# Kernel optimization log

Measured on AMD Instinct MI355X. Metric: run time of the kernel, lower is better.

## Reference

```python
import jax, jax.numpy as jnp
import numpy as np

B = 1
DIM = 2048
N_HEADS = 16
HEAD_DIM = 128
RANK = 128
ALPHA = 128.0
L_NOISE = 2048
L_COND = 1024
N_LORAS = 1
EPS = 1e-6
NEG = -1e20


def setup_inputs() -> dict:
    key = jax.random.key(0)
    ks = jax.random.split(key, 24)
    inp = {}
    inp["noise_flat"] = jax.random.normal(ks[0], (B, L_NOISE, DIM), jnp.float32)
    inp["cond_flat"] = jax.random.normal(ks[1], (B, L_COND, DIM), jnp.float32)
    # RoPE freqs in TE 'bshd' convention: (L, head_dim), halves duplicated
    inv_freq = 1.0 / (10000.0 ** (jnp.arange(0, HEAD_DIM, 2, dtype=jnp.float32) / HEAD_DIM))
    pos = jnp.arange(L_NOISE + L_COND, dtype=jnp.float32)
    fr = pos[:, None] * inv_freq[None, :]
    fr = jnp.concatenate([fr, fr], axis=-1)  # (L, HEAD_DIM)
    inp["noise_rope"] = fr[:L_NOISE]
    inp["cond_rope"] = fr[L_NOISE:]
    std = 0.02
    inp["Wq"] = jax.random.normal(ks[2], (DIM, DIM), jnp.float32) * std
    inp["Wk"] = jax.random.normal(ks[3], (DIM, DIM), jnp.float32) * std
    inp["Wv"] = jax.random.normal(ks[4], (DIM, DIM), jnp.float32) * std
    inp["Wo"] = jax.random.normal(ks[5], (DIM, DIM), jnp.float32) * std
    inp["bq"] = jnp.zeros((DIM,), jnp.float32)
    inp["bk"] = jnp.zeros((DIM,), jnp.float32)
    inp["bv"] = jnp.zeros((DIM,), jnp.float32)
    inp["bo"] = jnp.zeros((DIM,), jnp.float32)
    inp["q_norm_scale"] = jnp.ones((HEAD_DIM,), jnp.float32)
    inp["k_norm_scale"] = jnp.ones((HEAD_DIM,), jnp.float32)
    inp["v_norm_scale"] = jnp.ones((HEAD_DIM,), jnp.float32)
    # LoRA: down ~ N(0, 1/rank); up small nonzero (torch inits zeros, made nonzero for a meaningful baseline)
    for name, ki in zip(["q", "k", "v", "o"], range(6, 10)):
        k1, k2 = jax.random.split(ks[ki])
        inp[f"lora_{name}_down"] = jax.random.normal(k1, (DIM, RANK), jnp.float32) / RANK
        inp[f"lora_{name}_up"] = jax.random.normal(k2, (RANK, DIM), jnp.float32) * 0.01
    return inp


def _rms_norm(x, scale):
    return x * jax.lax.rsqrt(jnp.mean(x * x, axis=-1, keepdims=True) + EPS) * scale


def _rotate_half(x):
    x1, x2 = jnp.split(x, 2, axis=-1)
    return jnp.concatenate([-x2, x1], axis=-1)


def _apply_rope(x, freqs):
    # x: (B, L, H, D), freqs: (L, D)
    cos = jnp.cos(freqs)[None, :, None, :]
    sin = jnp.sin(freqs)[None, :, None, :]
    return x * cos + _rotate_half(x) * sin


def _block_mask():
    # noise rows attend to everything; cond block i attends only to itself
    L = L_NOISE + L_COND * N_LORAS
    idx = jnp.arange(L)
    is_noise = idx < L_NOISE
    blk = (idx - L_NOISE) // L_COND
    allowed = is_noise[:, None] | (
        (~is_noise[:, None]) & (~is_noise[None, :]) & (blk[:, None] == blk[None, :])
    )
    return jnp.where(allowed, 0.0, NEG).astype(jnp.float32)  # (L, L)


def _cond_mask(i, L):
    idx = jnp.arange(L)
    start = L_NOISE + i * L_COND
    return ((idx >= start) & (idx < start + L_COND)).astype(jnp.float32)[None, :, None]


def reference(noise_flat, cond_flat, noise_rope, cond_rope,
              Wq, Wk, Wv, Wo, bq, bk, bv, bo,
              q_norm_scale, k_norm_scale, v_norm_scale,
              lora_q_down, lora_q_up, lora_k_down, lora_k_up,
              lora_v_down, lora_v_up, lora_o_down, lora_o_up):
    joint = jnp.concatenate([noise_flat, cond_flat], axis=1)  # (B, L, D)
    rope = jnp.concatenate([noise_rope, cond_rope], axis=0)   # (L, HEAD_DIM)
    L = joint.shape[1]
    scale_lora = ALPHA / RANK
    m = _cond_mask(0, L)  # n_loras = 1, lora_weight = 1.0
    jm = joint * m

    def lora(x_masked, Wd, Wu):
        return (x_masked @ Wd) @ Wu * scale_lora

    q = joint @ Wq + bq + lora(jm, lora_q_down, lora_q_up)
    k = joint @ Wk + bk + lora(jm, lora_k_down, lora_k_up)
    v = joint @ Wv + bv + lora(jm, lora_v_down, lora_v_up)

    q = q.reshape(B, L, N_HEADS, HEAD_DIM)
    k = k.reshape(B, L, N_HEADS, HEAD_DIM)
    v = v.reshape(B, L, N_HEADS, HEAD_DIM)
    q = _rms_norm(q, q_norm_scale)
    k = _rms_norm(k, k_norm_scale)
    v = _rms_norm(v, v_norm_scale)
    q = _apply_rope(q, rope)
    k = _apply_rope(k, rope)

    bias = _block_mask()[None, None]  # (1,1,L,L)
    scores = jnp.einsum('bqhd,bkhd->bhqk', q, k) / jnp.sqrt(jnp.float32(HEAD_DIM)) + bias
    attn = jax.nn.softmax(scores, axis=-1)
    x = jnp.einsum('bhqk,bkhd->bqhd', attn, v).reshape(B, L, DIM)

    out = x @ Wo + bo + lora(x * m, lora_o_down, lora_o_up)
    return out[:, :L_NOISE, :], out[:, L_NOISE:, :]
```

## Files before the change

### kernel.cpp

```cpp
#include <hip/hip_runtime.h>

typedef _Float16 f16;
typedef _Float16 half8 __attribute__((ext_vector_type(8)));
typedef float floatx4 __attribute__((ext_vector_type(4)));

#define L_TOT   3072
#define L_NZ    2048
#define DIM_C   2048
#define NH      16
#define HD      128

__device__ __forceinline__ void gl_lds16(const f16* g, f16* l) {
    __builtin_amdgcn_global_load_lds((__attribute__((address_space(1))) void*)g,
                                     (__attribute__((address_space(3))) void*)l,
                                     16, 0, 0);
}

__global__ void sentinel_kernel(float* out) { out[0] = 1.0e6f; }

__global__ __launch_bounds__(256)
void cast_joint(const float* __restrict__ noise, const float* __restrict__ cond,
                f16* __restrict__ out) {
    int i = (blockIdx.x * 256 + threadIdx.x) * 4;
    const float* src; int off;
    if (i < 2048 * 2048) { src = noise; off = i; }
    else                 { src = cond;  off = i - 2048 * 2048; }
    float4 v = *(const float4*)(src + off);
    out[i+0] = (f16)v.x; out[i+1] = (f16)v.y;
    out[i+2] = (f16)v.z; out[i+3] = (f16)v.w;
}

__global__ __launch_bounds__(256)
void transpose_cast4(const float* __restrict__ s0, const float* __restrict__ s1,
                     const float* __restrict__ s2, const float* __restrict__ s3,
                     f16* __restrict__ dstBase, int R, int C, long long outBatch) {
    const float* in = (blockIdx.z == 0) ? s0 : (blockIdx.z == 1) ? s1 : (blockIdx.z == 2) ? s2 : s3;
    f16* out = dstBase + (long long)blockIdx.z * outBatch;
    __shared__ f16 tile[32][33];
    int x = threadIdx.x & 31, y0 = threadIdx.x >> 5;
    int r0 = blockIdx.y * 32, c0 = blockIdx.x * 32;
#pragma unroll
    for (int i = 0; i < 4; ++i) {
        int y = y0 + i * 8;
        tile[y][x] = (f16)in[(size_t)(r0 + y) * C + (c0 + x)];
    }
    __syncthreads();
#pragma unroll
    for (int i = 0; i < 4; ++i) {
        int y = y0 + i * 8;
        out[(size_t)(c0 + y) * R + (r0 + x)] = tile[x][y];
    }
}

template<int WRITE_HALF, int ACCUM, int ADD_BIAS, int MODE>
__global__ __launch_bounds__(256, 2)
void gemm_tn(const f16* __restrict__ A, const f16* __restrict__ BT,
             void* __restrict__ Cv,
             const float* __restrict__ bias0,
             int M, int N, int K, int lda, int ldb, int ldc) {
    __shared__ __align__(16) f16 lds[2][2][128 * 64];
    const int tid  = threadIdx.x;
    const int lane = tid & 63, wave = tid >> 6;
    const int m0 = blockIdx.y * 128, n0 = blockIdx.x * 128;
    const int wr = wave >> 1, wc = wave & 1;
    floatx4 acc[4][4] = {};

    if (MODE == 2) A += (size_t)(n0 >> 11) * 128;

    const int r0i = tid >> 3;
    const int gch = (tid & 7) ^ (r0i & 7);
    const f16* gA0 = A  + (size_t)(m0 + r0i) * lda + gch * 8;
    const f16* gB0 = BT + (size_t)(n0 + r0i) * ldb + gch * 8;
    const int ldsW = wave * 512;

    auto stage = [&](int buf, int k0) {
#pragma unroll
        for (int is = 0; is < 4; ++is)
            gl_lds16(gA0 + k0 + (size_t)is * 32 * lda, &lds[buf][0][0] + is * 2048 + ldsW);
#pragma unroll
        for (int is = 0; is < 4; ++is)
            gl_lds16(gB0 + k0 + (size_t)is * 32 * ldb, &lds[buf][1][0] + is * 2048 + ldsW);
    };

    const int rl = lane & 15, cq = lane >> 4;

    const int nIter = K >> 6;
    stage(0, 0);
    int cur = 0;
    for (int t = 0; t < nIter; ++t) {
        const int k0n = (t + 1 < nIter) ? (t + 1) * 64 : 0;
        stage(cur ^ 1, k0n);
        asm volatile("s_waitcnt vmcnt(8)" ::: "memory");
        __builtin_amdgcn_s_barrier();
        __builtin_amdgcn_sched_barrier(0);
#pragma unroll
        for (int kh = 0; kh < 2; ++kh) {
            half8 af[4], bf[4];
#pragma unroll
            for (int m = 0; m < 4; ++m) {
                int row = wr * 64 + m * 16 + rl;
                int pos = (kh * 4 + cq) ^ (row & 7);
                af[m] = *(const half8*)(&lds[cur][0][row * 64 + pos * 8]);
            }
#pragma unroll
            for (int n = 0; n < 4; ++n) {
                int row = wc * 64 + n * 16 + rl;
                int pos = (kh * 4 + cq) ^ (row & 7);
                bf[n] = *(const half8*)(&lds[cur][1][row * 64 + pos * 8]);
            }
#pragma unroll
            for (int m = 0; m < 4; ++m)
#pragma unroll
                for (int n = 0; n < 4; ++n)
                    acc[m][n] = __builtin_amdgcn_mfma_f32_16x16x32_f16(af[m], bf[n], acc[m][n], 0, 0, 0);
        }
        __builtin_amdgcn_s_barrier();
        __builtin_amdgcn_sched_barrier(0);
        cur ^= 1;
    }

    const int rq = lane >> 4;
    size_t cbase = 0;
    if (MODE == 2) cbase = (size_t)(n0 >> 11) * ((size_t)L_TOT * DIM_C);
#pragma unroll
    for (int m = 0; m < 4; ++m) {
        int row = m0 + wr * 64 + m * 16 + rq * 4;
#pragma unroll
        for (int n = 0; n < 4; ++n) {
            int col = n0 + wc * 64 + n * 16 + rl;
            int ccol = (MODE == 2) ? (col & 2047) : col;
            float badd = ADD_BIAS ? bias0[ccol] : 0.0f;
#pragma unroll
            for (int j = 0; j < 4; ++j) {
                float v = acc[m][n][j] + badd;
                size_t idx = cbase + (size_t)(row + j) * ldc + ccol;
                if (WRITE_HALF) {
                    f16* C = (f16*)Cv;
                    if (ACCUM) v += (float)C[idx];
                    C[idx] = (f16)v;
                } else {
                    float* C = (float*)Cv;
                    if (ACCUM) v += C[idx];
                    C[idx] = v;
                }
            }
        }
    }
}

__global__ __launch_bounds__(256, 2)
void gemm_pair(int nb0, int nbx0,
               const f16* __restrict__ A0, const f16* __restrict__ BT0, void* C0,
               const float* __restrict__ b00, const float* __restrict__ b01, const float* __restrict__ b02,
               int lda0, int ldb0, int ldc0, int wh0, int ab0, int mode0,
               int nbx1,
               const f16* __restrict__ A1, const f16* __restrict__ BT1, void* C1,
               int lda1, int ldb1, int ldc1, int wh1,
               int K) {
    __shared__ __align__(16) f16 lds[2][2][128 * 64];
    const int tid  = threadIdx.x;
    const int lane = tid & 63, wave = tid >> 6;
    const int bid = blockIdx.x;
    const bool j0 = (bid < nb0);
    const int lb  = j0 ? bid : (bid - nb0);
    const int nbx = j0 ? nbx0 : nbx1;
    const int bx = lb % nbx, by = lb / nbx;
    const int m0 = by * 128, n0 = bx * 128;
    const f16* A  = j0 ? A0  : A1;
    const f16* BT = j0 ? BT0 : BT1;
    const int lda = j0 ? lda0 : lda1, ldb = j0 ? ldb0 : ldb1, ldc = j0 ? ldc0 : ldc1;
    const int wr = wave >> 1, wc = wave & 1;
    floatx4 acc[4][4] = {};

    const int r0i = tid >> 3;
    const int gch = (tid & 7) ^ (r0i & 7);
    const f16* gA0 = A  + (size_t)(m0 + r0i) * lda + gch * 8;
    const f16* gB0 = BT + (size_t)(n0 + r0i) * ldb + gch * 8;
    const int ldsW = wave * 512;

    auto stage = [&](int buf, int k0) {
#pragma unroll
        for (int is = 0; is < 4; ++is)
            gl_lds16(gA0 + k0 + (size_t)is * 32 * lda, &lds[buf][0][0] + is * 2048 + ldsW);
#pragma unroll
        for (int is = 0; is < 4; ++is)
            gl_lds16(gB0 + k0 + (size_t)is * 32 * ldb, &lds[buf][1][0] + is * 2048 + ldsW);
    };

    const int rl = lane & 15, cq = lane >> 4;
    const int nIter = K >> 6;
    stage(0, 0);
    int cur = 0;
    for (int t = 0; t < nIter; ++t) {
        const int k0n = (t + 1 < nIter) ? (t + 1) * 64 : 0;
        stage(cur ^ 1, k0n);
        asm volatile("s_waitcnt vmcnt(8)" ::: "memory");
        __builtin_amdgcn_s_barrier();
        __builtin_amdgcn_sched_barrier(0);
#pragma unroll
        for (int kh = 0; kh < 2; ++kh) {
            half8 af[4], bf[4];
#pragma unroll
            for (int m = 0; m < 4; ++m) {
                int row = wr * 64 + m * 16 + rl;
                int pos = (kh * 4 + cq) ^ (row & 7);
                af[m] = *(const half8*)(&lds[cur][0][row * 64 + pos * 8]);
            }
#pragma unroll
            for (int n = 0; n < 4; ++n) {
                int row = wc * 64 + n * 16 + rl;
                int pos = (kh * 4 + cq) ^ (row & 7);
                bf[n] = *(const half8*)(&lds[cur][1][row * 64 + pos * 8]);
            }
#pragma unroll
            for (int m = 0; m < 4; ++m)
#pragma unroll
                for (int n = 0; n < 4; ++n)
                    acc[m][n] = __builtin_amdgcn_mfma_f32_16x16x32_f16(af[m], bf[n], acc[m][n], 0, 0, 0);
        }
        __builtin_amdgcn_s_barrier();
        __builtin_amdgcn_sched_barrier(0);
        cur ^= 1;
    }

    const int rq = lane >> 4;
    const int wh = j0 ? wh0 : wh1;
    const int ab = j0 ? ab0 : 0;
    const int md = j0 ? mode0 : 0;
    void* Cv = j0 ? C0 : C1;
    size_t cbase = 0;
    const float* bias = b00;
    if (md == 1) {
        int chunk = n0 >> 11;
        bias = (chunk == 0) ? b00 : ((chunk == 1) ? b01 : b02);
        cbase = (size_t)chunk * ((size_t)L_TOT * DIM_C);
    }
#pragma unroll
    for (int m = 0; m < 4; ++m) {
        int row = m0 + wr * 64 + m * 16 + rq * 4;
#pragma unroll
        for (int n = 0; n < 4; ++n) {
            int col = n0 + wc * 64 + n * 16 + rl;
            int ccol = (md == 1) ? (col & 2047) : col;
            float badd = ab ? bias[ccol] : 0.0f;
#pragma unroll
            for (int j = 0; j < 4; ++j) {
                float v = acc[m][n][j] + badd;
                size_t idx = cbase + (size_t)(row + j) * ldc + ccol;
                if (wh) ((f16*)Cv)[idx] = (f16)v;
                else    ((float*)Cv)[idx] = v;
            }
        }
    }
}

__global__ __launch_bounds__(256)
void norm_rope_v(const f16* __restrict__ q16, const f16* __restrict__ k16, const f16* __restrict__ v16,
                 const float* __restrict__ qs, const float* __restrict__ ks, const float* __restrict__ vs,
                 const float* __restrict__ nrope, const float* __restrict__ crope,
                 f16* __restrict__ qH, f16* __restrict__ kH, f16* __restrict__ vT) {
    __shared__ f16 vtile[128][33];
    const int t = threadIdx.x, rloc = t >> 3, c = t & 7;
    const int r = blockIdx.x * 32 + rloc, h = blockIdx.y;
    const int d0 = c * 8;
    const size_t src = (size_t)r * DIM_C + h * HD;
    half8 qlv = *(const half8*)(q16 + src + d0);
    half8 qhv = *(const half8*)(q16 + src + 64 + d0);
    half8 klv = *(const half8*)(k16 + src + d0);
    half8 khv = *(const half8*)(k16 + src + 64 + d0);
    half8 vlv = *(const half8*)(v16 + src + d0);
    half8 vhv = *(const half8*)(v16 + src + 64 + d0);
    float ql[8], qh[8], kl[8], kh[8], vl[8], vh[8];
    float sq = 0.f, sk = 0.f, sv = 0.f;
#pragma unroll
    for (int i = 0; i < 8; ++i) {
        ql[i] = (float)qlv[i]; qh[i] = (float)qhv[i];
        kl[i] = (float)klv[i]; kh[i] = (float)khv[i];
        vl[i] = (float)vlv[i]; vh[i] = (float)vhv[i];
        sq += ql[i]*ql[i] + qh[i]*qh[i];
        sk += kl[i]*kl[i] + kh[i]*kh[i];
        sv += vl[i]*vl[i] + vh[i]*vh[i];
    }
    sq += __shfl_xor(sq, 1); sq += __shfl_xor(sq, 2); sq += __shfl_xor(sq, 4);
    sk += __shfl_xor(sk, 1); sk += __shfl_xor(sk, 2); sk += __shfl_xor(sk, 4);
    sv += __shfl_xor(sv, 1); sv += __shfl_xor(sv, 2); sv += __shfl_xor(sv, 4);
    const float rqs = rsqrtf(sq * (1.0f / 128.0f) + 1e-6f);
    const float rks = rsqrtf(sk * (1.0f / 128.0f) + 1e-6f);
    const float rvs = rsqrtf(sv * (1.0f / 128.0f) + 1e-6f);
    const float* rp = (r < L_NZ) ? (nrope + (size_t)r * HD) : (crope + (size_t)(r - L_NZ) * HD);
    half8 qo_l, qo_h, ko_l, ko_h;
#pragma unroll
    for (int i = 0; i < 8; ++i) {
        float fr = rp[d0 + i];
        float cs = cosf(fr), sn = sinf(fr);
        float qnl = ql[i] * rqs * qs[d0 + i],      qnh = qh[i] * rqs * qs[64 + d0 + i];
        float knl = kl[i] * rks * ks[d0 + i],      knh = kh[i] * rks * ks[64 + d0 + i];
        qo_l[i] = (f16)((qnl * cs - qnh * sn) * 0.08838834764831845f);
        qo_h[i] = (f16)((qnh * cs + qnl * sn) * 0.08838834764831845f);
        ko_l[i] = (f16)(knl * cs - knh * sn);
        ko_h[i] = (f16)(knh * cs + knl * sn);
        vtile[d0 + i][rloc]      = (f16)(vl[i] * rvs * vs[d0 + i]);
        vtile[64 + d0 + i][rloc] = (f16)(vh[i] * rvs * vs[64 + d0 + i]);
    }
    const size_t dst = ((size_t)h * L_TOT + r) * HD;
    *(half8*)(qH + dst + d0) = qo_l;      *(half8*)(qH + dst + 64 + d0) = qo_h;
    *(half8*)(kH + dst + d0) = ko_l;      *(half8*)(kH + dst + 64 + d0) = ko_h;
    __syncthreads();
    const int dd = t >> 1, seg = (t & 1) * 16;
    half8 o0, o1;
#pragma unroll
    for (int i = 0; i < 8; ++i) { o0[i] = vtile[dd][seg + i]; o1[i] = vtile[dd][seg + 8 + i]; }
    f16* vdst = vT + ((size_t)h * HD + dd) * L_TOT + blockIdx.x * 32 + seg;
    *(half8*)(vdst)     = o0;
    *(half8*)(vdst + 8) = o1;
}

__global__ __launch_bounds__(256, 2)
void flash_kernel(const f16* __restrict__ qH, const f16* __restrict__ kH,
                  const f16* __restrict__ vT, f16* __restrict__ xH) {
    __shared__ __align__(16) f16 lds_k[2][64 * 128];
    __shared__ __align__(16) f16 lds_v[64 * 128];
    __shared__ __align__(16) f16 p_lds[4][16][72];
    const int tid = threadIdx.x;
    const int lane = tid & 63, w = tid >> 6;
    const int bid = blockIdx.x;
    const int xcd = bid & 7, rr = bid >> 3;
    int h, qb;
    if (rr < 32) { h = xcd + 8 * (rr >> 4); qb = 32 + (rr & 15); }
    else         { int li = rr - 32; h = xcd + 8 * (li >> 5); qb = li & 31; }
    const int q0 = qb * 64 + w * 16;
    const int rl = lane & 15, rq = lane >> 4;

    half8 aq[4];
    const f16* qbase = qH + ((size_t)h * L_TOT + q0) * HD;
#pragma unroll
    for (int kc = 0; kc < 4; ++kc)
        aq[kc] = *(const half8*)(qbase + (size_t)rl * HD + kc * 32 + rq * 8);

    floatx4 acc[8] = {};
    floatx4 accl = {};
    const half8 vone = {(f16)1.f, (f16)1.f, (f16)1.f, (f16)1.f,
                        (f16)1.f, (f16)1.f, (f16)1.f, (f16)1.f};

    const int kLo = (qb >= 32) ? L_NZ : 0;
    const f16* khead = kH + (size_t)h * L_TOT * HD;
    const f16* vhead = vT + (size_t)h * HD * L_TOT;

    auto stageK = [&](int kb, int pb) {
#pragma unroll
        for (int is = 0; is < 4; ++is) {
            int i = is * 256 + tid;
            int r = i >> 4, c = i & 15;
            gl_lds16(khead + (size_t)(kb + r) * HD + ((c ^ (r & 15)) * 8),
                     &lds_k[pb][0] + (is * 256 + w * 64) * 8);
        }
    };
    auto stageV = [&](int kb) {
#pragma unroll
        for (int is = 0; is < 4; ++is) {
            int i = is * 256 + tid;
            int pair = i >> 4, c10 = i & 15;
            int g10 = c10 ^ (pair & 15);
            int d = pair * 2 + (g10 >> 3), kchunk = g10 & 7;
            gl_lds16(vhead + (size_t)d * L_TOT + kb + kchunk * 8,
                     lds_v + (is * 256 + w * 64) * 8);
        }
    };

    asm volatile("s_waitcnt vmcnt(0)" ::: "memory");
    stageK(kLo, 0);
    int p = 0;
    for (int kb = kLo; kb < L_TOT; kb += 64) {
        const int kbn = (kb + 64 < L_TOT) ? (kb + 64) : kLo;
        stageV(kb);
        stageK(kbn, p ^ 1);
        asm volatile("s_waitcnt vmcnt(8)" ::: "memory");
        __builtin_amdgcn_s_barrier();
        __builtin_amdgcn_sched_barrier(0);

        const f16* kbase = &lds_k[p][0];
        floatx4 sacc[4] = {};
        __builtin_amdgcn_s_setprio(1);
#pragma unroll
        for (int kf = 0; kf < 4; ++kf) {
            int r = kf * 16 + rl;
#pragma unroll
            for (int kc = 0; kc < 4; ++kc) {
                half8 bk = *(const half8*)(kbase + r * 128 + (((kc * 4 + rq) ^ (r & 15)) * 8));
                sacc[kf] = __builtin_amdgcn_mfma_f32_16x16x32_f16(aq[kc], bk, sacc[kf], 0, 0, 0);
            }
        }
        __builtin_amdgcn_s_setprio(0);
#pragma unroll
        for (int kf = 0; kf < 4; ++kf)
#pragma unroll
            for (int j = 0; j < 4; ++j) {
                float pv = __expf(sacc[kf][j] - 4.0f);
                p_lds[w][rq * 4 + j][kf * 16 + rl] = (f16)pv;
            }

        asm volatile("s_waitcnt vmcnt(4)" ::: "memory");
        __builtin_amdgcn_s_barrier();
        __builtin_amdgcn_sched_barrier(0);

        __builtin_amdgcn_s_setprio(1);
#pragma unroll
        for (int kc = 0; kc < 2; ++kc) {
            half8 ap = *(const half8*)(&p_lds[w][rl][kc * 32 + rq * 8]);
            accl = __builtin_amdgcn_mfma_f32_16x16x32_f16(ap, vone, accl, 0, 0, 0);
#pragma unroll
            for (int dt = 0; dt < 8; ++dt) {
                int d = dt * 16 + rl;
                int g10 = (d & 1) * 8 + kc * 4 + rq;
                half8 bv = *(const half8*)(lds_v + (d >> 1) * 128 + ((g10 ^ ((d >> 1) & 15)) * 8));
                acc[dt] = __builtin_amdgcn_mfma_f32_16x16x32_f16(ap, bv, acc[dt], 0, 0, 0);
            }
        }
        __builtin_amdgcn_s_setprio(0);
        __builtin_amdgcn_s_barrier();
        p ^= 1;
    }

#pragma unroll
    for (int j = 0; j < 4; ++j) {
        float li = 1.0f / accl[j];
        int row = q0 + rq * 4 + j;
#pragma unroll
        for (int dt = 0; dt < 8; ++dt)
            xH[(size_t)row * DIM_C + h * HD + dt * 16 + rl] = (f16)(acc[dt][j] * li);
    }
}

extern "C" void kernel_launch(void* const* d_in, const int* in_sizes, int n_in,
                              void* d_out, int out_size, void* d_ws, size_t ws_size,
                              hipStream_t stream) {
    const float* noise = (const float*)d_in[0];
    const float* cond  = (const float*)d_in[1];
    const float* nrope = (const float*)d_in[2];
    const float* crope = (const float*)d_in[3];
    const float* Wq = (const float*)d_in[4];
    const float* Wk = (const float*)d_in[5];
    const float* Wv = (const float*)d_in[6];
    const float* Wo = (const float*)d_in[7];
    const float* bq = (const float*)d_in[8];
    const float* bk = (const float*)d_in[9];
    const float* bv = (const float*)d_in[10];
    const float* bo = (const float*)d_in[11];
    const float* qs = (const float*)d_in[12];
    const float* ks = (const float*)d_in[13];
    const float* vs = (const float*)d_in[14];
    const float* lqd = (const float*)d_in[15];
    const float* lqu = (const float*)d_in[16];
    const float* lkd = (const float*)d_in[17];
    const float* lku = (const float*)d_in[18];
    const float* lvd = (const float*)d_in[19];
    const float* lvu = (const float*)d_in[20];
    const float* lod = (const float*)d_in[21];
    const float* lou = (const float*)d_in[22];
    (void)in_sizes; (void)n_in; (void)out_size;

    char* ws = (char*)d_ws;
    const size_t SZ_LD = (size_t)L_TOT * DIM_C * sizeof(f16);
    const size_t SZ_W  = (size_t)DIM_C * DIM_C * sizeof(f16);
    size_t o = 0;
    auto take = [&](size_t b) { size_t r = o; o += (b + 255) & ~(size_t)255; return r; };
    f16* jointH = (f16*)(ws + take(SZ_LD));
    f16* WTqkv  = (f16*)(ws + take(4 * SZ_W));
    f16* WT3    = WTqkv + (size_t)3 * 2048 * 2048;
    f16* downT  = (f16*)(ws + take((size_t)4 * 128 * 2048 * 2));
    f16* downTo = downT + (size_t)3 * 128 * 2048;
    f16* upT    = (f16*)(ws + take((size_t)4 * 2048 * 128 * 2));
    f16* upTo   = upT + (size_t)3 * 2048 * 128;
    f16* q16    = (f16*)(ws + take(3 * SZ_LD));
    f16* k16    = q16 + (size_t)L_TOT * DIM_C;
    f16* v16    = k16 + (size_t)L_TOT * DIM_C;
    f16* t_all  = (f16*)(ws + take((size_t)1024 * 384 * 2));
    f16* t_o    = (f16*)(ws + take((size_t)1024 * 128 * 2));
    f16* qHd    = (f16*)(ws + take(SZ_LD));
    f16* kHd    = (f16*)(ws + take(SZ_LD));
    f16* vTd    = (f16*)(ws + take(SZ_LD));
    f16* xH     = (f16*)(ws + take(SZ_LD));
    if (o > ws_size) {
        sentinel_kernel<<<1, 1, 0, stream>>>((float*)d_out);
        return;
    }

    cast_joint<<<dim3(6144), 256, 0, stream>>>(noise, cond, jointH);
    transpose_cast4<<<dim3(64, 64, 4), 256, 0, stream>>>(Wq, Wk, Wv, Wo, WTqkv, 2048, 2048,
                                                         (long long)2048 * 2048);
    transpose_cast4<<<dim3(4, 64, 4), 256, 0, stream>>>(lqd, lkd, lvd, lod, downT, 2048, 128,
                                                        (long long)128 * 2048);
    transpose_cast4<<<dim3(64, 4, 4), 256, 0, stream>>>(lqu, lku, lvu, lou, upT, 128, 2048,
                                                        (long long)2048 * 128);

    gemm_pair<<<dim3(1152 + 24), 256, 0, stream>>>(
        1152, 48, jointH, WTqkv, q16, bq, bk, bv, 2048, 2048, 2048, 1, 1, 1,
        3, jointH + (size_t)2048 * 2048, downT, t_all, 2048, 2048, 384, 1,
        2048);
    gemm_tn<1, 1, 0, 2><<<dim3(48, 8), 256, 0, stream>>>(t_all, upT, q16 + (size_t)2048 * 2048,
                                                         nullptr, 1024, 6144, 128, 384, 128, 2048);

    norm_rope_v<<<dim3(96, 16), 256, 0, stream>>>(q16, k16, v16, qs, ks, vs, nrope, crope,
                                                  qHd, kHd, vTd);

    flash_kernel<<<dim3(768), 256, 0, stream>>>(qHd, kHd, vTd, xH);

    gemm_pair<<<dim3(384 + 8), 256, 0, stream>>>(
        384, 16, xH, WT3, d_out, bo, nullptr, nullptr, 2048, 2048, 2048, 0, 1, 0,
        1, xH + (size_t)2048 * 2048, downTo, t_o, 2048, 2048, 128, 1,
        2048);
    gemm_tn<0, 1, 0, 0><<<dim3(16, 8), 256, 0, stream>>>(t_o, upTo, (float*)d_out + (size_t)2048 * 2048,
                                                         nullptr, 1024, 2048, 128, 128, 128, 2048);
}
```

Before: 338.4 us.

## Split noise-query attention over key ranges with partial outputs and a combine pass

The flash kernel now splits each noise query block's 3072-key range into three 1024-key slices. Each slice is handled by a separate workgroup, which writes a normalized partial output and its row sum. A new combine kernel merges the slices. Workgroups grow to 512 threads covering 128 query rows, with 32-key tiles and smaller LDS buffers, to balance the noise and cond workloads and raise occupancy. This adds a partial-output write and read through workspace (reusing the q16 buffer) and an extra launch, and it halves the per-iteration MFMA work relative to the sync overhead.

```diff
diff --git a/kernel.cpp b/kernel.cpp
--- a/kernel.cpp
+++ b/kernel.cpp
@@ -315,20 +315,25 @@
     *(half8*)(vdst + 8) = o1;
 }
 
-__global__ __launch_bounds__(256, 2)
+__global__ __launch_bounds__(512, 8)
 void flash_kernel(const f16* __restrict__ qH, const f16* __restrict__ kH,
-                  const f16* __restrict__ vT, f16* __restrict__ xH) {
-    __shared__ __align__(16) f16 lds_k[2][64 * 128];
-    __shared__ __align__(16) f16 lds_v[64 * 128];
-    __shared__ __align__(16) f16 p_lds[4][16][72];
+                  const f16* __restrict__ vT, f16* __restrict__ xH,
+                  f16* __restrict__ Opart, float* __restrict__ lpart) {
+    __shared__ __align__(16) f16 lds_k[2][32 * 128];
+    __shared__ __align__(16) f16 lds_v[64 * 64];
+    __shared__ __align__(16) f16 p_lds[8][16][40];
     const int tid = threadIdx.x;
     const int lane = tid & 63, w = tid >> 6;
     const int bid = blockIdx.x;
     const int xcd = bid & 7, rr = bid >> 3;
-    int h, qb;
-    if (rr < 32) { h = xcd + 8 * (rr >> 4); qb = 32 + (rr & 15); }
-    else         { int li = rr - 32; h = xcd + 8 * (li >> 5); qb = li & 31; }
-    const int q0 = qb * 64 + w * 16;
+    const int h = xcd + 8 * (rr / 56);
+    const int s = rr % 56;
+    const bool isNoise = (s < 48);
+    const int qb  = isNoise ? (s / 3) : (16 + (s - 48));
+    const int sl  = isNoise ? (s % 3) : 0;
+    const int kLo = isNoise ? sl * 1024 : L_NZ;
+    const int kHi = kLo + 1024;
+    const int q0 = qb * 128 + w * 16;
     const int rl = lane & 15, rq = lane >> 4;
 
     half8 aq[4];
@@ -342,47 +347,38 @@
     const half8 vone = {(f16)1.f, (f16)1.f, (f16)1.f, (f16)1.f,
                         (f16)1.f, (f16)1.f, (f16)1.f, (f16)1.f};
 
-    const int kLo = (qb >= 32) ? L_NZ : 0;
     const f16* khead = kH + (size_t)h * L_TOT * HD;
     const f16* vhead = vT + (size_t)h * HD * L_TOT;
 
     auto stageK = [&](int kb, int pb) {
-#pragma unroll
-        for (int is = 0; is < 4; ++is) {
-            int i = is * 256 + tid;
-            int r = i >> 4, c = i & 15;
-            gl_lds16(khead + (size_t)(kb + r) * HD + ((c ^ (r & 15)) * 8),
-                     &lds_k[pb][0] + (is * 256 + w * 64) * 8);
-        }
+        int r = tid >> 4, c = tid & 15;
+        gl_lds16(khead + (size_t)(kb + r) * HD + ((c ^ (r & 15)) * 8),
+                 &lds_k[pb][0] + tid * 8);
     };
     auto stageV = [&](int kb) {
-#pragma unroll
-        for (int is = 0; is < 4; ++is) {
-            int i = is * 256 + tid;
-            int pair = i >> 4, c10 = i & 15;
-            int g10 = c10 ^ (pair & 15);
-            int d = pair * 2 + (g10 >> 3), kchunk = g10 & 7;
-            gl_lds16(vhead + (size_t)d * L_TOT + kb + kchunk * 8,
-                     lds_v + (is * 256 + w * 64) * 8);
-        }
+        int pair = tid >> 3, c3 = tid & 7;
+        int g3 = c3 ^ (pair & 7);
+        int d = pair * 2 + (g3 >> 2), kchunk = g3 & 3;
+        gl_lds16(vhead + (size_t)d * L_TOT + kb + kchunk * 8,
+                 lds_v + tid * 8);
     };
 
     asm volatile("s_waitcnt vmcnt(0)" ::: "memory");
     stageK(kLo, 0);
     int p = 0;
-    for (int kb = kLo; kb < L_TOT; kb += 64) {
-        const int kbn = (kb + 64 < L_TOT) ? (kb + 64) : kLo;
+    for (int kb = kLo; kb < kHi; kb += 32) {
+        const int kbn = (kb + 32 < kHi) ? (kb + 32) : kLo;
         stageV(kb);
         stageK(kbn, p ^ 1);
-        asm volatile("s_waitcnt vmcnt(8)" ::: "memory");
+        asm volatile("s_waitcnt vmcnt(2)" ::: "memory");
         __builtin_amdgcn_s_barrier();
         __builtin_amdgcn_sched_barrier(0);
 
         const f16* kbase = &lds_k[p][0];
-        floatx4 sacc[4] = {};
+        floatx4 sacc[2] = {};
         __builtin_amdgcn_s_setprio(1);
 #pragma unroll
-        for (int kf = 0; kf < 4; ++kf) {
+        for (int kf = 0; kf < 2; ++kf) {
             int r = kf * 16 + rl;
 #pragma unroll
             for (int kc = 0; kc < 4; ++kc) {
@@ -392,43 +388,77 @@
         }
         __builtin_amdgcn_s_setprio(0);
 #pragma unroll
-        for (int kf = 0; kf < 4; ++kf)
+        for (int kf = 0; kf < 2; ++kf)
 #pragma unroll
             for (int j = 0; j < 4; ++j) {
                 float pv = __expf(sacc[kf][j] - 4.0f);
                 p_lds[w][rq * 4 + j][kf * 16 + rl] = (f16)pv;
             }
 
-        asm volatile("s_waitcnt vmcnt(4)" ::: "memory");
+        asm volatile("s_waitcnt vmcnt(1)" ::: "memory");
         __builtin_amdgcn_s_barrier();
         __builtin_amdgcn_sched_barrier(0);
 
+        half8 ap = *(const half8*)(&p_lds[w][rl][rq * 8]);
         __builtin_amdgcn_s_setprio(1);
-#pragma unroll
-        for (int kc = 0; kc < 2; ++kc) {
-            half8 ap = *(const half8*)(&p_lds[w][rl][kc * 32 + rq * 8]);
-            accl = __builtin_amdgcn_mfma_f32_16x16x32_f16(ap, vone, accl, 0, 0, 0);
-#pragma unroll
-            for (int dt = 0; dt < 8; ++dt) {
-                int d = dt * 16 + rl;
-                int g10 = (d & 1) * 8 + kc * 4 + rq;
-                half8 bv = *(const half8*)(lds_v + (d >> 1) * 128 + ((g10 ^ ((d >> 1) & 15)) * 8));
-                acc[dt] = __builtin_amdgcn_mfma_f32_16x16x32_f16(ap, bv, acc[dt], 0, 0, 0);
-            }
+        accl = __builtin_amdgcn_mfma_f32_16x16x32_f16(ap, vone, accl, 0, 0, 0);
+#pragma unroll
+        for (int dt = 0; dt < 8; ++dt) {
+            int d = dt * 16 + rl;
+            int pair = d >> 1;
+            int g3 = (d & 1) * 4 + rq;
+            half8 bv = *(const half8*)(lds_v + pair * 64 + ((g3 ^ (pair & 7)) * 8));
+            acc[dt] = __builtin_amdgcn_mfma_f32_16x16x32_f16(ap, bv, acc[dt], 0, 0, 0);
         }
         __builtin_amdgcn_s_setprio(0);
         __builtin_amdgcn_s_barrier();
         p ^= 1;
     }
 
-#pragma unroll
-    for (int j = 0; j < 4; ++j) {
-        float li = 1.0f / accl[j];
-        int row = q0 + rq * 4 + j;
-#pragma unroll
-        for (int dt = 0; dt < 8; ++dt)
-            xH[(size_t)row * DIM_C + h * HD + dt * 16 + rl] = (f16)(acc[dt][j] * li);
-    }
+    if (isNoise) {
+        f16* op = Opart + ((size_t)sl * NH + h) * ((size_t)L_NZ * HD);
+        float* lp = lpart + ((size_t)sl * NH + h) * L_NZ;
+#pragma unroll
+        for (int j = 0; j < 4; ++j) {
+            float li = 1.0f / accl[j];
+            int row = q0 + rq * 4 + j;
+            if (rl == 0) lp[row] = accl[j];
+#pragma unroll
+            for (int dt = 0; dt < 8; ++dt)
+                op[(size_t)row * HD + dt * 16 + rl] = (f16)(acc[dt][j] * li);
+        }
+    } else {
+#pragma unroll
+        for (int j = 0; j < 4; ++j) {
+            float li = 1.0f / accl[j];
+            int row = q0 + rq * 4 + j;
+#pragma unroll
+            for (int dt = 0; dt < 8; ++dt)
+                xH[(size_t)row * DIM_C + h * HD + dt * 16 + rl] = (f16)(acc[dt][j] * li);
+        }
+    }
+}
+
+__global__ __launch_bounds__(256)
+void combine_noise(const f16* __restrict__ Opart, const float* __restrict__ lpart,
+                   f16* __restrict__ xH) {
+    const size_t PS = (size_t)NH * L_NZ * HD;
+    const int t = threadIdx.x, lr = t >> 4, dc = t & 15;
+    const int R = blockIdx.x * 16 + lr;
+    const int h = R >> 11, q = R & 2047;
+    const float l0 = lpart[(size_t)0 * NH * L_NZ + (size_t)h * L_NZ + q];
+    const float l1 = lpart[(size_t)1 * NH * L_NZ + (size_t)h * L_NZ + q];
+    const float l2 = lpart[(size_t)2 * NH * L_NZ + (size_t)h * L_NZ + q];
+    const float inv = 1.0f / (l0 + l1 + l2);
+    const size_t base = ((size_t)h * L_NZ + q) * HD + dc * 8;
+    half8 a = *(const half8*)(Opart + 0 * PS + base);
+    half8 b = *(const half8*)(Opart + 1 * PS + base);
+    half8 c = *(const half8*)(Opart + 2 * PS + base);
+    half8 out;
+#pragma unroll
+    for (int i = 0; i < 8; ++i)
+        out[i] = (f16)((l0 * (float)a[i] + l1 * (float)b[i] + l2 * (float)c[i]) * inv);
+    *(half8*)(xH + (size_t)q * DIM_C + h * HD + dc * 8) = out;
 }
 
 extern "C" void kernel_launch(void* const* d_in, const int* in_sizes, int n_in,
@@ -480,6 +510,8 @@
     f16* kHd    = (f16*)(ws + take(SZ_LD));
     f16* vTd    = (f16*)(ws + take(SZ_LD));
     f16* xH     = (f16*)(ws + take(SZ_LD));
+    f16*   Opart = q16;
+    float* lpart = (float*)(q16 + (size_t)3 * NH * L_NZ * HD);
     if (o > ws_size) {
         sentinel_kernel<<<1, 1, 0, stream>>>((float*)d_out);
         return;
@@ -503,7 +535,8 @@
     norm_rope_v<<<dim3(96, 16), 256, 0, stream>>>(q16, k16, v16, qs, ks, vs, nrope, crope,
                                                   qHd, kHd, vTd);
 
-    flash_kernel<<<dim3(768), 256, 0, stream>>>(qHd, kHd, vTd, xH);
+    flash_kernel<<<dim3(896), 512, 0, stream>>>(qHd, kHd, vTd, xH, Opart, lpart);
+    combine_noise<<<dim3(2048), 256, 0, stream>>>(Opart, lpart, xH);
 
     gemm_pair<<<dim3(384 + 8), 256, 0, stream>>>(
         384, 16, xH, WT3, d_out, bo, nullptr, nullptr, 2048, 2048, 2048, 0, 1, 0,
```

After: 608.7 us. 1.8x slower.
